# Performance work log

Hardware: AMD Instinct MI355X
Metric: run time of the kernel (lower is better)

Reference implementation:

```python
import jax, jax.numpy as jnp
import numpy as np

N_HEAD = 8
HEAD_DIM = 64
DIM = 512
INNER = N_HEAD * HEAD_DIM
ATT_THRESHOLD = 1e-4
SCALE = HEAD_DIM ** -0.5


def setup_inputs() -> dict:
    key = jax.random.key(0)
    ks = jax.random.split(key, 7)
    b, n, dn = 2, 2048, 2048
    fr = jax.random.normal(ks[0], (b, n, DIM), dtype=jnp.float32)
    dt = jax.random.normal(ks[1], (b, dn, DIM), dtype=jnp.float32)
    s = DIM ** -0.5
    Wq = jax.random.normal(ks[2], (DIM, INNER), dtype=jnp.float32) * s
    Wk = jax.random.normal(ks[3], (DIM, INNER), dtype=jnp.float32) * s
    Wv = jax.random.normal(ks[4], (DIM, INNER), dtype=jnp.float32) * s
    Wo = jax.random.normal(ks[5], (INNER, DIM), dtype=jnp.float32) * (INNER ** -0.5)
    bo = jax.random.normal(ks[6], (DIM,), dtype=jnp.float32) * 0.01
    return {"fr": fr, "dt": dt, "Wq": Wq, "Wk": Wk, "Wv": Wv, "Wo": Wo, "bo": bo}


def reference(fr, dt, Wq, Wk, Wv, Wo, bo):
    b, n, _ = fr.shape
    dn = dt.shape[1]
    # projections -> [b, seq, n_head, head_dim]
    q = (fr @ Wq).reshape(b, n, N_HEAD, HEAD_DIM)
    k = (dt @ Wk).reshape(b, dn, N_HEAD, HEAD_DIM)
    v = (dt @ Wv).reshape(b, dn, N_HEAD, HEAD_DIM)
    # full attention matrix [b, h, n, dn]
    scores = jnp.einsum('bihd,bjhd->bhij', q, k) * SCALE
    attn = jax.nn.softmax(scores, axis=-1)
    # torch .clip(t) with one positional arg clamps the MIN: max(attn, t)
    attn = jnp.maximum(attn, ATT_THRESHOLD) - ATT_THRESHOLD
    attn = attn / jnp.sum(attn, axis=-1, keepdims=True)
    out = jnp.einsum('bhij,bjhd->bihd', attn, v).reshape(b, n, INNER)
    return out @ Wo + bo
```

## Files before the change

kernel.cpp:

```cpp
#include <hip/hip_runtime.h>
#include <hip/hip_bf16.h>

#define BB 2
#define SEQ 2048
#define NHEAD 8
#define HD 64
#define ATT_T 1e-4f
#define QSCALE 0.18033688011112042f

typedef short s16x8 __attribute__((ext_vector_type(8)));
typedef float f32x16 __attribute__((ext_vector_type(16)));

#define MFMA32(a, b, c) __builtin_amdgcn_mfma_f32_32x32x16_bf16((a), (b), (c), 0, 0, 0)
#define EXP2(x) __builtin_amdgcn_exp2f(x)
#define SB0() __builtin_amdgcn_sched_barrier(0)
#define WAITVM0() __builtin_amdgcn_s_waitcnt(0x0F70)
#define WAITVM4() __builtin_amdgcn_s_waitcnt(0x0F74)
#define WAITVM8() __builtin_amdgcn_s_waitcnt(0x0F78)

__device__ __forceinline__ unsigned short bfr(float x) {
  __hip_bfloat16 h = __float2bfloat16(x);
  return __builtin_bit_cast(unsigned short, h);
}
__device__ __forceinline__ unsigned int packbf(float a, float b) {
  return (unsigned int)bfr(a) | ((unsigned int)bfr(b) << 16);
}
__device__ __forceinline__ unsigned int permpack(float a, float b) {
  return __builtin_amdgcn_perm(__builtin_bit_cast(unsigned int, b),
                               __builtin_bit_cast(unsigned int, a), 0x07060302u);
}
__device__ __forceinline__ void async16(const void* g, void* l) {
  __builtin_amdgcn_global_load_lds(
      (const __attribute__((address_space(1))) unsigned int*)g,
      (__attribute__((address_space(3))) unsigned int*)l, 16, 0, 0);
}

__global__ __launch_bounds__(256) void prep(const float* __restrict__ fr,
                                            const float* __restrict__ dt,
                                            const float* __restrict__ w0,
                                            const float* __restrict__ w1,
                                            const float* __restrict__ w2,
                                            const float* __restrict__ w3,
                                            unsigned short* __restrict__ frB,
                                            unsigned short* __restrict__ dtB,
                                            unsigned short* __restrict__ o0,
                                            unsigned short* __restrict__ o1,
                                            unsigned short* __restrict__ o2,
                                            unsigned short* __restrict__ o3) {
  __shared__ float tle[64][65];
  const int bid = blockIdx.x;
  if (bid < 4096) {
    const float* x = bid < 2048 ? fr : dt;
    unsigned short* y = bid < 2048 ? frB : dtB;
    size_t i = ((size_t)(bid & 2047) * 256 + threadIdx.x) * 4;
    float4 v = *(const float4*)(x + i);
    uint2 p;
    p.x = packbf(v.x, v.y);
    p.y = packbf(v.z, v.w);
    *(uint2*)(y + i) = p;
    return;
  }
  const int idx = bid - 4096;
  const int z = idx >> 6;
  const float* W = z == 0 ? w0 : z == 1 ? w1 : z == 2 ? w2 : w3;
  unsigned short* WT = z == 0 ? o0 : z == 1 ? o1 : z == 2 ? o2 : o3;
  const int r0 = ((idx >> 3) & 7) * 64, c0 = (idx & 7) * 64;
  const int tr = threadIdx.x >> 4;
  const int tc = threadIdx.x & 15;
  #pragma unroll
  for (int i = 0; i < 4; i++) {
    int r = tr + i * 16;
    float4 v = *(const float4*)(W + (size_t)(r0 + r) * 512 + c0 + tc * 4);
    tle[r][tc * 4 + 0] = v.x;
    tle[r][tc * 4 + 1] = v.y;
    tle[r][tc * 4 + 2] = v.z;
    tle[r][tc * 4 + 3] = v.w;
  }
  __syncthreads();
  #pragma unroll
  for (int i = 0; i < 4; i++) {
    int c = tr + i * 16;
    int rr = tc * 4;
    uint2 p;
    p.x = packbf(tle[rr + 0][c], tle[rr + 1][c]);
    p.y = packbf(tle[rr + 2][c], tle[rr + 3][c]);
    *(uint2*)(WT + (size_t)(c0 + c) * 512 + r0 + rr) = p;
  }
}

__device__ __forceinline__ void gemm_core_bk64(const unsigned short* __restrict__ A,
                                               const unsigned short* __restrict__ BT,
                                               unsigned short* smem, int m0, int n0,
                                               int w, int lane, f32x16 (&acc)[2]) {
  unsigned short* Asm = smem;
  unsigned short* Bsm = smem + 8192;
  const int l31 = lane & 31, lh = lane >> 5;

  auto stage = [&](int kt, int buf) {
    const int k0 = kt * 64;
    #pragma unroll
    for (int i = 0; i < 2; i++) {
      int r = w * 2 + i, g = r >> 2, ks = r & 3;
      async16(A + (size_t)(m0 + g * 32 + l31) * 512 + k0 + ks * 16 + lh * 8,
              Asm + buf * 4096 + r * 512);
    }
    #pragma unroll
    for (int i = 0; i < 4; i++) {
      int r = w * 4 + i, gn = r >> 2, ks = r & 3;
      async16(BT + (size_t)(n0 + gn * 32 + l31) * 512 + k0 + ks * 16 + lh * 8,
              Bsm + buf * 8192 + r * 512);
    }
  };

  stage(0, 0);
  for (int kt = 0; kt < 8; ++kt) {
    __syncthreads();
    if (kt + 1 < 8) stage(kt + 1, (kt + 1) & 1);
    const int buf = kt & 1;
    const unsigned short* as = Asm + buf * 4096 + (w & 1) * 2048;
    const unsigned short* bs = Bsm + buf * 8192 + (w >> 1) * 4096;
    #pragma unroll
    for (int ks = 0; ks < 4; ++ks) {
      s16x8 af = *(const s16x8*)(as + ks * 512 + lane * 8);
      s16x8 b0 = *(const s16x8*)(bs + ks * 512 + lane * 8);
      s16x8 b1 = *(const s16x8*)(bs + 2048 + ks * 512 + lane * 8);
      acc[0] = MFMA32(af, b0, acc[0]);
      acc[1] = MFMA32(af, b1, acc[1]);
    }
  }
}

__global__ __launch_bounds__(256) void gemm_qkv(const unsigned short* __restrict__ frB,
                                                const unsigned short* __restrict__ dtB,
                                                const unsigned short* __restrict__ WqT,
                                                const unsigned short* __restrict__ WkT,
                                                const unsigned short* __restrict__ WvT,
                                                unsigned short* __restrict__ Qp,
                                                unsigned short* __restrict__ Kp,
                                                unsigned short* __restrict__ VTp) {
  __shared__ __align__(16) unsigned short smem[24576];
  const int tid = threadIdx.x, lane = tid & 63, w = tid >> 6;
  const int l31 = lane & 31, lh = lane >> 5;
  const int m0 = blockIdx.y * 64, n0 = blockIdx.x * 128;
  const int z = blockIdx.z;
  const unsigned short* A = z == 0 ? frB : dtB;
  const unsigned short* BT = z == 0 ? WqT : (z == 1 ? WkT : WvT);
  unsigned short* OP = z == 0 ? Qp : (z == 1 ? Kp : VTp);
  const float scale = z == 0 ? QSCALE : 1.0f;

  f32x16 acc[2];
  #pragma unroll
  for (int j = 0; j < 2; j++)
    #pragma unroll
    for (int r = 0; r < 16; r++) acc[j][r] = 0.f;

  gemm_core_bk64(A, BT, smem, m0, n0, w, lane, acc);

  const int wm = (w & 1) * 32, wn = (w >> 1) * 64;
  const int bb = m0 >> 11, s0 = m0 & 2047;
  __syncthreads();
  if (z <= 1) {
    #pragma unroll
    for (int j = 0; j < 2; j++)
      #pragma unroll
      for (int r = 0; r < 16; r++) {
        int mm = wm + (r & 3) + 8 * (r >> 2) + 4 * lh;
        int nn = wn + j * 32 + l31;
        smem[mm * 136 + nn] = bfr(acc[j][r] * scale);
      }
    __syncthreads();
    #pragma unroll
    for (int it = 0; it < 4; ++it) {
      int c = tid + it * 256;
      int mm = c >> 4, seg = c & 15;
      uint4 vdat = *(const uint4*)(smem + mm * 136 + seg * 8);
      int n = n0 + seg * 8, h = n >> 6, d = n & 63;
      *(uint4*)(OP + ((size_t)((bb * NHEAD + h) * SEQ + s0 + mm)) * HD + d) = vdat;
    }
  } else {
    #pragma unroll
    for (int j = 0; j < 2; j++)
      #pragma unroll
      for (int r = 0; r < 16; r += 2) {
        int mm = wm + (r & 3) + 8 * (r >> 2) + 4 * lh;
        int nn = wn + j * 32 + l31;
        *(unsigned int*)(smem + nn * 72 + mm) = packbf(acc[j][r], acc[j][r + 1]);
      }
    __syncthreads();
    #pragma unroll
    for (int it = 0; it < 4; ++it) {
      int c = tid + it * 256;
      int nn = c >> 3, seg = c & 7;
      uint4 vdat = *(const uint4*)(smem + nn * 72 + seg * 8);
      int n = n0 + nn, h = n >> 6, d = n & 63;
      *(uint4*)(OP + ((size_t)((bb * NHEAD + h) * HD + d)) * SEQ + s0 + seg * 8) = vdat;
    }
  }
}

__global__ __launch_bounds__(256) void gemm_out(const unsigned short* __restrict__ A,
                                                const unsigned short* __restrict__ BT,
                                                const float* __restrict__ bias,
                                                float* __restrict__ O) {
  __shared__ __align__(16) unsigned short smem[24576];
  const int tid = threadIdx.x, lane = tid & 63, w = tid >> 6;
  const int l31 = lane & 31, lh = lane >> 5;
  const int m0 = blockIdx.y * 64, n0 = blockIdx.x * 128;

  f32x16 acc[2];
  #pragma unroll
  for (int j = 0; j < 2; j++)
    #pragma unroll
    for (int r = 0; r < 16; r++) acc[j][r] = 0.f;

  gemm_core_bk64(A, BT, smem, m0, n0, w, lane, acc);

  const int wm = (w & 1) * 32, wn = (w >> 1) * 64;
  #pragma unroll
  for (int j = 0; j < 2; j++) {
    float bv = bias[n0 + wn + j * 32 + l31];
    #pragma unroll
    for (int r = 0; r < 16; r++) {
      int mm = wm + (r & 3) + 8 * (r >> 2) + 4 * lh;
      O[(size_t)(m0 + mm) * 512 + n0 + wn + j * 32 + l31] = acc[j][r] + bv;
    }
  }
}

__global__ __launch_bounds__(256, 2) void attn_mfma(const unsigned short* __restrict__ Q,
                                                    const unsigned short* __restrict__ K,
                                                    const unsigned short* __restrict__ VT,
                                                    unsigned short* __restrict__ O) {
  __shared__ __align__(16) unsigned short arena[4][8192];
  __shared__ float larr[4][64];
  __shared__ float warr[4][64];

  const int tid = threadIdx.x;
  const int lane = tid & 63;
  const int w = tid >> 6;
  const int l31 = lane & 31, lh = lane >> 5;

  const int bid = blockIdx.x;
  const int g = bid & 7, j = bid >> 3;
  const int bh = g * 2 + (j >> 5);
  const int qt = j & 31;

  const unsigned short* Qh = Q + (size_t)bh * SEQ * HD;
  const unsigned short* Kh = K + (size_t)bh * SEQ * HD;
  const unsigned short* VTh = VT + (size_t)bh * HD * SEQ;

  s16x8 qf[2][4];
  #pragma unroll
  for (int q2 = 0; q2 < 2; q2++)
    #pragma unroll
    for (int t = 0; t < 4; t++)
      qf[q2][t] = *(const s16x8*)(Qh + (size_t)(qt * 64 + q2 * 32 + l31) * HD + 16 * t + 8 * lh);

  unsigned short* kbuf = &arena[w][0];
  unsigned short* vbuf = &arena[w][4096];
  const int kbase = w * 512;

  auto stageK = [&](int c, int slot) {
    const unsigned short* base = Kh + (size_t)(kbase + c * 32 + l31) * HD + lh * 8;
    #pragma unroll
    for (int tt = 0; tt < 4; tt++)
      async16(base + tt * 16, kbuf + slot * 2048 + tt * 512);
  };
  auto stageV = [&](int c, int slot) {
    #pragma unroll
    for (int dh = 0; dh < 2; dh++)
      #pragma unroll
      for (int kc = 0; kc < 2; kc++)
        async16(VTh + (size_t)(dh * 32 + l31) * SEQ + kbase + c * 32 + kc * 16 + lh * 8,
                vbuf + slot * 2048 + (dh * 2 + kc) * 512);
  };

  float lsum[2] = {0.f, 0.f};
  f32x16 scp[2];

  auto accum_l = [&]() {
    #pragma unroll
    for (int q2 = 0; q2 < 2; q2++) {
      float s0 = 0.f, s1 = 0.f, s2 = 0.f, s3 = 0.f;
      #pragma unroll
      for (int r = 0; r < 4; r++) {
        s0 += EXP2(scp[q2][r]);
        s1 += EXP2(scp[q2][4 + r]);
        s2 += EXP2(scp[q2][8 + r]);
        s3 += EXP2(scp[q2][12 + r]);
      }
      lsum[q2] += (s0 + s1) + (s2 + s3);
    }
  };

  stageK(0, 0);
  for (int c = 0; c < 16; ++c) {
    const int slot = c & 1;
    if (c + 1 < 16) stageK(c + 1, slot ^ 1);
    if (c > 0) accum_l();
    if (c + 1 < 16) { WAITVM4(); } else { WAITVM0(); }
    SB0();
    s16x8 kf[4];
    #pragma unroll
    for (int tt = 0; tt < 4; tt++)
      kf[tt] = *(const s16x8*)(kbuf + slot * 2048 + tt * 512 + lane * 8);
    #pragma unroll
    for (int q2 = 0; q2 < 2; q2++) {
      f32x16 sc;
      #pragma unroll
      for (int r = 0; r < 16; r++) sc[r] = 0.f;
      #pragma unroll
      for (int tt = 0; tt < 4; tt++) sc = MFMA32(kf[tt], qf[q2][tt], sc);
      scp[q2] = sc;
    }
  }
  accum_l();
  #pragma unroll
  for (int q2 = 0; q2 < 2; q2++) lsum[q2] += __shfl_xor(lsum[q2], 32);
  if (lh == 0) { larr[w][l31] = lsum[0]; larr[w][32 + l31] = lsum[1]; }
  __syncthreads();
  float tl[2];
  #pragma unroll
  for (int q2 = 0; q2 < 2; q2++)
    tl[q2] = ATT_T * (larr[0][q2 * 32 + l31] + larr[1][q2 * 32 + l31] +
                      larr[2][q2 * 32 + l31] + larr[3][q2 * 32 + l31]);

  f32x16 acc[2][2];
  #pragma unroll
  for (int q2 = 0; q2 < 2; q2++)
    #pragma unroll
    for (int dh = 0; dh < 2; dh++)
      #pragma unroll
      for (int r = 0; r < 16; r++) acc[q2][dh][r] = 0.f;
  float wacc[2] = {0.f, 0.f};
  s16x8 vfp[2][2];

  auto softmax_pv = [&]() {
    s16x8 pf[2][2];
    #pragma unroll
    for (int q2 = 0; q2 < 2; q2++) {
      uint2 quads[4];
      #pragma unroll
      for (int gq = 0; gq < 4; gq++) {
        float u0 = fmaxf(EXP2(scp[q2][4 * gq + 0]) - tl[q2], 0.f);
        float u1 = fmaxf(EXP2(scp[q2][4 * gq + 1]) - tl[q2], 0.f);
        float u2 = fmaxf(EXP2(scp[q2][4 * gq + 2]) - tl[q2], 0.f);
        float u3 = fmaxf(EXP2(scp[q2][4 * gq + 3]) - tl[q2], 0.f);
        wacc[q2] += (u0 + u1) + (u2 + u3);
        quads[gq].x = permpack(u0, u1);
        quads[gq].y = permpack(u2, u3);
      }
      #pragma unroll
      for (int tp = 0; tp < 2; tp++) {
        uint2 ea, eb;
        ea.x = (unsigned)__shfl_xor((int)quads[2 * tp].x, 32);
        ea.y = (unsigned)__shfl_xor((int)quads[2 * tp].y, 32);
        eb.x = (unsigned)__shfl_xor((int)quads[2 * tp + 1].x, 32);
        eb.y = (unsigned)__shfl_xor((int)quads[2 * tp + 1].y, 32);
        uint4 fr;
        if (lh == 0) { fr.x = quads[2 * tp].x; fr.y = quads[2 * tp].y; fr.z = ea.x; fr.w = ea.y; }
        else         { fr.x = eb.x; fr.y = eb.y; fr.z = quads[2 * tp + 1].x; fr.w = quads[2 * tp + 1].y; }
        pf[q2][tp] = __builtin_bit_cast(s16x8, fr);
      }
    }
    #pragma unroll
    for (int q2 = 0; q2 < 2; q2++)
      #pragma unroll
      for (int dh = 0; dh < 2; dh++) {
        acc[q2][dh] = MFMA32(pf[q2][0], vfp[dh][0], acc[q2][dh]);
        acc[q2][dh] = MFMA32(pf[q2][1], vfp[dh][1], acc[q2][dh]);
      }
  };

  stageK(0, 0);
  stageV(0, 0);
  for (int c = 0; c < 16; ++c) {
    const int slot = c & 1;
    if (c + 1 < 16) { stageK(c + 1, slot ^ 1); stageV(c + 1, slot ^ 1); }
    if (c > 0) softmax_pv();
    if (c + 1 < 16) { WAITVM8(); } else { WAITVM0(); }
    SB0();
    s16x8 kf[4];
    #pragma unroll
    for (int tt = 0; tt < 4; tt++)
      kf[tt] = *(const s16x8*)(kbuf + slot * 2048 + tt * 512 + lane * 8);
    #pragma unroll
    for (int dh = 0; dh < 2; dh++)
      #pragma unroll
      for (int kc = 0; kc < 2; kc++)
        vfp[dh][kc] = *(const s16x8*)(vbuf + slot * 2048 + (dh * 2 + kc) * 512 + lane * 8);
    #pragma unroll
    for (int q2 = 0; q2 < 2; q2++) {
      f32x16 sc;
      #pragma unroll
      for (int r = 0; r < 16; r++) sc[r] = 0.f;
      #pragma unroll
      for (int tt = 0; tt < 4; tt++) sc = MFMA32(kf[tt], qf[q2][tt], sc);
      scp[q2] = sc;
    }
  }
  softmax_pv();

  #pragma unroll
  for (int q2 = 0; q2 < 2; q2++) wacc[q2] += __shfl_xor(wacc[q2], 32);
  if (lh == 0) { warr[w][l31] = wacc[0]; warr[w][32 + l31] = wacc[1]; }
  __syncthreads();

  float* plane0 = (float*)&arena[0][0];
  float* plane1 = (float*)&arena[2][0];

  if (w >= 2) {
    float* pl = (w == 2) ? plane0 : plane1;
    #pragma unroll
    for (int q2 = 0; q2 < 2; q2++)
      #pragma unroll
      for (int dh = 0; dh < 2; dh++)
        #pragma unroll
        for (int r = 0; r < 16; r++) {
          int ql = q2 * 32 + (r & 3) + 8 * (r >> 2) + 4 * lh;
          pl[ql * 64 + dh * 32 + l31] = acc[q2][dh][r];
        }
  }
  __syncthreads();
  if (w < 2) {
    float* pl = (w == 0) ? plane0 : plane1;
    #pragma unroll
    for (int q2 = 0; q2 < 2; q2++)
      #pragma unroll
      for (int dh = 0; dh < 2; dh++)
        #pragma unroll
        for (int r = 0; r < 16; r++) {
          int ql = q2 * 32 + (r & 3) + 8 * (r >> 2) + 4 * lh;
          acc[q2][dh][r] += pl[ql * 64 + dh * 32 + l31];
        }
  }
  __syncthreads();
  if (w == 1) {
    #pragma unroll
    for (int q2 = 0; q2 < 2; q2++)
      #pragma unroll
      for (int dh = 0; dh < 2; dh++)
        #pragma unroll
        for (int r = 0; r < 16; r++) {
          int ql = q2 * 32 + (r & 3) + 8 * (r >> 2) + 4 * lh;
          plane0[ql * 64 + dh * 32 + l31] = acc[q2][dh][r];
        }
  }
  __syncthreads();
  unsigned short* otile = &arena[2][0];
  if (w == 0) {
    #pragma unroll
    for (int q2 = 0; q2 < 2; q2++)
      #pragma unroll
      for (int dh = 0; dh < 2; dh++)
        #pragma unroll
        for (int r = 0; r < 16; r++) {
          int ql = q2 * 32 + (r & 3) + 8 * (r >> 2) + 4 * lh;
          float wt = warr[0][ql] + warr[1][ql] + warr[2][ql] + warr[3][ql];
          float v = (acc[q2][dh][r] + plane0[ql * 64 + dh * 32 + l31]) / wt;
          otile[ql * 64 + dh * 32 + l31] = bfr(v);
        }
  }
  __syncthreads();
  const int b = bh >> 3, h = bh & 7;
  #pragma unroll
  for (int it = 0; it < 2; ++it) {
    int c2 = tid + it * 256;
    int mm = c2 >> 3, seg = c2 & 7;
    uint4 vdat = *(const uint4*)(otile + mm * 64 + seg * 8);
    *(uint4*)(O + ((size_t)(b * SEQ + qt * 64 + mm)) * 512 + h * HD + seg * 8) = vdat;
  }
}

extern "C" void kernel_launch(void* const* d_in, const int* in_sizes, int n_in,
                              void* d_out, int out_size, void* d_ws, size_t ws_size,
                              hipStream_t stream) {
  const float* fr = (const float*)d_in[0];
  const float* dt = (const float*)d_in[1];
  const float* Wq = (const float*)d_in[2];
  const float* Wk = (const float*)d_in[3];
  const float* Wv = (const float*)d_in[4];
  const float* Wo = (const float*)d_in[5];
  const float* bo = (const float*)d_in[6];
  float* out = (float*)d_out;

  const size_t planeE = (size_t)BB * SEQ * 512;
  const size_t wE = 512 * 512;
  unsigned short* p = (unsigned short*)d_ws;
  unsigned short* frB = p; p += planeE;
  unsigned short* dtB = p; p += planeE;
  unsigned short* WqT = p; p += wE;
  unsigned short* WkT = p; p += wE;
  unsigned short* WvT = p; p += wE;
  unsigned short* WoT = p; p += wE;
  unsigned short* Qp  = p; p += planeE;
  unsigned short* Kp  = p; p += planeE;
  unsigned short* VTp = p; p += planeE;
  unsigned short* aoB = p; p += planeE;

  prep<<<4352, 256, 0, stream>>>(fr, dt, Wq, Wk, Wv, Wo, frB, dtB, WqT, WkT, WvT, WoT);

  gemm_qkv<<<dim3(4, 64, 3), 256, 0, stream>>>(frB, dtB, WqT, WkT, WvT, Qp, Kp, VTp);

  attn_mfma<<<BB * NHEAD * 32, 256, 0, stream>>>(Qp, Kp, VTp, aoB);

  gemm_out<<<dim3(4, 64), 256, 0, stream>>>(aoB, WoT, bo, out);
}
```

Baseline: 166.1 us.

## Cache exp scores in registers as bf16 to skip recomputing QK^T in second pass

The attention kernel now computes QK^T and exp2 only once. It packs the exponentials as bf16 into a 128-register array and reuses them in the second pass, which previously reloaded K and redid the score MFMAs. The query tile per block drops from 64 to 32 rows, which doubles the grid and halves LDS use. This raises register pressure sharply and may hurt occupancy or cause spills. Rounding to bf16 before the threshold subtraction also changes numerics slightly.

```diff
diff --git a/kernel.cpp b/kernel.cpp
--- a/kernel.cpp
+++ b/kernel.cpp
@@ -16,7 +16,6 @@
 #define SB0() __builtin_amdgcn_sched_barrier(0)
 #define WAITVM0() __builtin_amdgcn_s_waitcnt(0x0F70)
 #define WAITVM4() __builtin_amdgcn_s_waitcnt(0x0F74)
-#define WAITVM8() __builtin_amdgcn_s_waitcnt(0x0F78)
 
 __device__ __forceinline__ unsigned short bfr(float x) {
   __hip_bfloat16 h = __float2bfloat16(x);
@@ -28,6 +27,12 @@
 __device__ __forceinline__ unsigned int permpack(float a, float b) {
   return __builtin_amdgcn_perm(__builtin_bit_cast(unsigned int, b),
                                __builtin_bit_cast(unsigned int, a), 0x07060302u);
+}
+__device__ __forceinline__ float unpack_lo(unsigned int p) {
+  return __builtin_bit_cast(float, p << 16);
+}
+__device__ __forceinline__ float unpack_hi(unsigned int p) {
+  return __builtin_bit_cast(float, p & 0xFFFF0000u);
 }
 __device__ __forceinline__ void async16(const void* g, void* l) {
   __builtin_amdgcn_global_load_lds(
@@ -231,9 +236,9 @@
                                                     const unsigned short* __restrict__ K,
                                                     const unsigned short* __restrict__ VT,
                                                     unsigned short* __restrict__ O) {
-  __shared__ __align__(16) unsigned short arena[4][8192];
-  __shared__ float larr[4][64];
-  __shared__ float warr[4][64];
+  __shared__ __align__(16) unsigned short arena[4][2][2048];
+  __shared__ float larr[4][32];
+  __shared__ float warr[4][32];
 
   const int tid = threadIdx.x;
   const int lane = tid & 63;
@@ -242,29 +247,25 @@
 
   const int bid = blockIdx.x;
   const int g = bid & 7, j = bid >> 3;
-  const int bh = g * 2 + (j >> 5);
-  const int qt = j & 31;
+  const int bh = g * 2 + (j >> 6);
+  const int qt = j & 63;
 
   const unsigned short* Qh = Q + (size_t)bh * SEQ * HD;
   const unsigned short* Kh = K + (size_t)bh * SEQ * HD;
   const unsigned short* VTh = VT + (size_t)bh * HD * SEQ;
 
-  s16x8 qf[2][4];
-  #pragma unroll
-  for (int q2 = 0; q2 < 2; q2++)
-    #pragma unroll
-    for (int t = 0; t < 4; t++)
-      qf[q2][t] = *(const s16x8*)(Qh + (size_t)(qt * 64 + q2 * 32 + l31) * HD + 16 * t + 8 * lh);
-
-  unsigned short* kbuf = &arena[w][0];
-  unsigned short* vbuf = &arena[w][4096];
+  s16x8 qf[4];
+  #pragma unroll
+  for (int t = 0; t < 4; t++)
+    qf[t] = *(const s16x8*)(Qh + (size_t)(qt * 32 + l31) * HD + 16 * t + 8 * lh);
+
   const int kbase = w * 512;
 
   auto stageK = [&](int c, int slot) {
     const unsigned short* base = Kh + (size_t)(kbase + c * 32 + l31) * HD + lh * 8;
     #pragma unroll
     for (int tt = 0; tt < 4; tt++)
-      async16(base + tt * 16, kbuf + slot * 2048 + tt * 512);
+      async16(base + tt * 16, &arena[w][slot][tt * 512]);
   };
   auto stageV = [&](int c, int slot) {
     #pragma unroll
@@ -272,203 +273,153 @@
       #pragma unroll
       for (int kc = 0; kc < 2; kc++)
         async16(VTh + (size_t)(dh * 32 + l31) * SEQ + kbase + c * 32 + kc * 16 + lh * 8,
-                vbuf + slot * 2048 + (dh * 2 + kc) * 512);
+                &arena[w][slot][(dh * 2 + kc) * 512]);
   };
 
-  float lsum[2] = {0.f, 0.f};
-  f32x16 scp[2];
-
-  auto accum_l = [&]() {
-    #pragma unroll
-    for (int q2 = 0; q2 < 2; q2++) {
-      float s0 = 0.f, s1 = 0.f, s2 = 0.f, s3 = 0.f;
-      #pragma unroll
-      for (int r = 0; r < 4; r++) {
-        s0 += EXP2(scp[q2][r]);
-        s1 += EXP2(scp[q2][4 + r]);
-        s2 += EXP2(scp[q2][8 + r]);
-        s3 += EXP2(scp[q2][12 + r]);
-      }
-      lsum[q2] += (s0 + s1) + (s2 + s3);
-    }
-  };
-
+  unsigned int P[16][8];
+
+  float ls0 = 0.f, ls1 = 0.f, ls2 = 0.f, ls3 = 0.f;
   stageK(0, 0);
+  #pragma unroll 16
   for (int c = 0; c < 16; ++c) {
     const int slot = c & 1;
     if (c + 1 < 16) stageK(c + 1, slot ^ 1);
-    if (c > 0) accum_l();
+    else stageV(0, 0);
+    WAITVM4();
+    SB0();
+    s16x8 kf[4];
+    #pragma unroll
+    for (int tt = 0; tt < 4; tt++)
+      kf[tt] = *(const s16x8*)&arena[w][slot][tt * 512 + lane * 8];
+    f32x16 sc;
+    #pragma unroll
+    for (int r = 0; r < 16; r++) sc[r] = 0.f;
+    #pragma unroll
+    for (int tt = 0; tt < 4; tt++) sc = MFMA32(kf[tt], qf[tt], sc);
+    #pragma unroll
+    for (int gq = 0; gq < 4; gq++) {
+      float e0 = EXP2(sc[4 * gq + 0]);
+      float e1 = EXP2(sc[4 * gq + 1]);
+      float e2 = EXP2(sc[4 * gq + 2]);
+      float e3 = EXP2(sc[4 * gq + 3]);
+      ls0 += e0; ls1 += e1; ls2 += e2; ls3 += e3;
+      P[c][2 * gq + 0] = permpack(e0, e1);
+      P[c][2 * gq + 1] = permpack(e2, e3);
+    }
+  }
+  float lsum = (ls0 + ls1) + (ls2 + ls3);
+  lsum += __shfl_xor(lsum, 32);
+  if (lh == 0) larr[w][l31] = lsum;
+  __syncthreads();
+  const float tl = ATT_T * (larr[0][l31] + larr[1][l31] + larr[2][l31] + larr[3][l31]);
+
+  f32x16 acc[2];
+  #pragma unroll
+  for (int dh = 0; dh < 2; dh++)
+    #pragma unroll
+    for (int r = 0; r < 16; r++) acc[dh][r] = 0.f;
+  float wacc = 0.f;
+
+  #pragma unroll 16
+  for (int c = 0; c < 16; ++c) {
+    const int slot = c & 1;
+    if (c + 1 < 16) stageV(c + 1, slot ^ 1);
+    uint2 quads[4];
+    #pragma unroll
+    for (int gq = 0; gq < 4; gq++) {
+      unsigned pa = P[c][2 * gq + 0], pb = P[c][2 * gq + 1];
+      float u0 = fmaxf(unpack_lo(pa) - tl, 0.f);
+      float u1 = fmaxf(unpack_hi(pa) - tl, 0.f);
+      float u2 = fmaxf(unpack_lo(pb) - tl, 0.f);
+      float u3 = fmaxf(unpack_hi(pb) - tl, 0.f);
+      wacc += (u0 + u1) + (u2 + u3);
+      quads[gq].x = permpack(u0, u1);
+      quads[gq].y = permpack(u2, u3);
+    }
+    s16x8 pf[2];
+    #pragma unroll
+    for (int tp = 0; tp < 2; tp++) {
+      unsigned sx = (lh == 0) ? quads[2 * tp + 1].x : quads[2 * tp].x;
+      unsigned sy = (lh == 0) ? quads[2 * tp + 1].y : quads[2 * tp].y;
+      unsigned rx = (unsigned)__shfl_xor((int)sx, 32);
+      unsigned ry = (unsigned)__shfl_xor((int)sy, 32);
+      uint4 fr;
+      if (lh == 0) { fr.x = quads[2 * tp].x; fr.y = quads[2 * tp].y; fr.z = rx; fr.w = ry; }
+      else         { fr.x = rx; fr.y = ry; fr.z = quads[2 * tp + 1].x; fr.w = quads[2 * tp + 1].y; }
+      pf[tp] = __builtin_bit_cast(s16x8, fr);
+    }
     if (c + 1 < 16) { WAITVM4(); } else { WAITVM0(); }
     SB0();
-    s16x8 kf[4];
-    #pragma unroll
-    for (int tt = 0; tt < 4; tt++)
-      kf[tt] = *(const s16x8*)(kbuf + slot * 2048 + tt * 512 + lane * 8);
-    #pragma unroll
-    for (int q2 = 0; q2 < 2; q2++) {
-      f32x16 sc;
-      #pragma unroll
-      for (int r = 0; r < 16; r++) sc[r] = 0.f;
-      #pragma unroll
-      for (int tt = 0; tt < 4; tt++) sc = MFMA32(kf[tt], qf[q2][tt], sc);
-      scp[q2] = sc;
-    }
-  }
-  accum_l();
-  #pragma unroll
-  for (int q2 = 0; q2 < 2; q2++) lsum[q2] += __shfl_xor(lsum[q2], 32);
-  if (lh == 0) { larr[w][l31] = lsum[0]; larr[w][32 + l31] = lsum[1]; }
-  __syncthreads();
-  float tl[2];
-  #pragma unroll
-  for (int q2 = 0; q2 < 2; q2++)
-    tl[q2] = ATT_T * (larr[0][q2 * 32 + l31] + larr[1][q2 * 32 + l31] +
-                      larr[2][q2 * 32 + l31] + larr[3][q2 * 32 + l31]);
-
-  f32x16 acc[2][2];
-  #pragma unroll
-  for (int q2 = 0; q2 < 2; q2++)
-    #pragma unroll
-    for (int dh = 0; dh < 2; dh++)
-      #pragma unroll
-      for (int r = 0; r < 16; r++) acc[q2][dh][r] = 0.f;
-  float wacc[2] = {0.f, 0.f};
-  s16x8 vfp[2][2];
-
-  auto softmax_pv = [&]() {
-    s16x8 pf[2][2];
-    #pragma unroll
-    for (int q2 = 0; q2 < 2; q2++) {
-      uint2 quads[4];
-      #pragma unroll
-      for (int gq = 0; gq < 4; gq++) {
-        float u0 = fmaxf(EXP2(scp[q2][4 * gq + 0]) - tl[q2], 0.f);
-        float u1 = fmaxf(EXP2(scp[q2][4 * gq + 1]) - tl[q2], 0.f);
-        float u2 = fmaxf(EXP2(scp[q2][4 * gq + 2]) - tl[q2], 0.f);
-        float u3 = fmaxf(EXP2(scp[q2][4 * gq + 3]) - tl[q2], 0.f);
-        wacc[q2] += (u0 + u1) + (u2 + u3);
-        quads[gq].x = permpack(u0, u1);
-        quads[gq].y = permpack(u2, u3);
-      }
-      #pragma unroll
-      for (int tp = 0; tp < 2; tp++) {
-        uint2 ea, eb;
-        ea.x = (unsigned)__shfl_xor((int)quads[2 * tp].x, 32);
-        ea.y = (unsigned)__shfl_xor((int)quads[2 * tp].y, 32);
-        eb.x = (unsigned)__shfl_xor((int)quads[2 * tp + 1].x, 32);
-        eb.y = (unsigned)__shfl_xor((int)quads[2 * tp + 1].y, 32);
-        uint4 fr;
-        if (lh == 0) { fr.x = quads[2 * tp].x; fr.y = quads[2 * tp].y; fr.z = ea.x; fr.w = ea.y; }
-        else         { fr.x = eb.x; fr.y = eb.y; fr.z = quads[2 * tp + 1].x; fr.w = quads[2 * tp + 1].y; }
-        pf[q2][tp] = __builtin_bit_cast(s16x8, fr);
-      }
-    }
-    #pragma unroll
-    for (int q2 = 0; q2 < 2; q2++)
-      #pragma unroll
-      for (int dh = 0; dh < 2; dh++) {
-        acc[q2][dh] = MFMA32(pf[q2][0], vfp[dh][0], acc[q2][dh]);
-        acc[q2][dh] = MFMA32(pf[q2][1], vfp[dh][1], acc[q2][dh]);
-      }
-  };
-
-  stageK(0, 0);
-  stageV(0, 0);
-  for (int c = 0; c < 16; ++c) {
-    const int slot = c & 1;
-    if (c + 1 < 16) { stageK(c + 1, slot ^ 1); stageV(c + 1, slot ^ 1); }
-    if (c > 0) softmax_pv();
-    if (c + 1 < 16) { WAITVM8(); } else { WAITVM0(); }
-    SB0();
-    s16x8 kf[4];
-    #pragma unroll
-    for (int tt = 0; tt < 4; tt++)
-      kf[tt] = *(const s16x8*)(kbuf + slot * 2048 + tt * 512 + lane * 8);
+    s16x8 vf[2][2];
     #pragma unroll
     for (int dh = 0; dh < 2; dh++)
       #pragma unroll
       for (int kc = 0; kc < 2; kc++)
-        vfp[dh][kc] = *(const s16x8*)(vbuf + slot * 2048 + (dh * 2 + kc) * 512 + lane * 8);
-    #pragma unroll
-    for (int q2 = 0; q2 < 2; q2++) {
-      f32x16 sc;
-      #pragma unroll
-      for (int r = 0; r < 16; r++) sc[r] = 0.f;
-      #pragma unroll
-      for (int tt = 0; tt < 4; tt++) sc = MFMA32(kf[tt], qf[q2][tt], sc);
-      scp[q2] = sc;
-    }
-  }
-  softmax_pv();
-
-  #pragma unroll
-  for (int q2 = 0; q2 < 2; q2++) wacc[q2] += __shfl_xor(wacc[q2], 32);
-  if (lh == 0) { warr[w][l31] = wacc[0]; warr[w][32 + l31] = wacc[1]; }
-  __syncthreads();
-
-  float* plane0 = (float*)&arena[0][0];
-  float* plane1 = (float*)&arena[2][0];
+        vf[dh][kc] = *(const s16x8*)&arena[w][slot][(dh * 2 + kc) * 512 + lane * 8];
+    #pragma unroll
+    for (int dh = 0; dh < 2; dh++) {
+      acc[dh] = MFMA32(pf[0], vf[dh][0], acc[dh]);
+      acc[dh] = MFMA32(pf[1], vf[dh][1], acc[dh]);
+    }
+  }
+
+  wacc += __shfl_xor(wacc, 32);
+  if (lh == 0) warr[w][l31] = wacc;
+  __syncthreads();
+
+  float* plane0 = (float*)&arena[0][0][0];
+  float* plane1 = (float*)&arena[1][0][0];
+  unsigned short* otile = &arena[2][0][0];
 
   if (w >= 2) {
     float* pl = (w == 2) ? plane0 : plane1;
     #pragma unroll
-    for (int q2 = 0; q2 < 2; q2++)
-      #pragma unroll
-      for (int dh = 0; dh < 2; dh++)
-        #pragma unroll
-        for (int r = 0; r < 16; r++) {
-          int ql = q2 * 32 + (r & 3) + 8 * (r >> 2) + 4 * lh;
-          pl[ql * 64 + dh * 32 + l31] = acc[q2][dh][r];
-        }
+    for (int dh = 0; dh < 2; dh++)
+      #pragma unroll
+      for (int r = 0; r < 16; r++) {
+        int ql = (r & 3) + 8 * (r >> 2) + 4 * lh;
+        pl[ql * 64 + dh * 32 + l31] = acc[dh][r];
+      }
   }
   __syncthreads();
   if (w < 2) {
     float* pl = (w == 0) ? plane0 : plane1;
     #pragma unroll
-    for (int q2 = 0; q2 < 2; q2++)
-      #pragma unroll
-      for (int dh = 0; dh < 2; dh++)
-        #pragma unroll
-        for (int r = 0; r < 16; r++) {
-          int ql = q2 * 32 + (r & 3) + 8 * (r >> 2) + 4 * lh;
-          acc[q2][dh][r] += pl[ql * 64 + dh * 32 + l31];
-        }
+    for (int dh = 0; dh < 2; dh++)
+      #pragma unroll
+      for (int r = 0; r < 16; r++) {
+        int ql = (r & 3) + 8 * (r >> 2) + 4 * lh;
+        acc[dh][r] += pl[ql * 64 + dh * 32 + l31];
+      }
   }
   __syncthreads();
   if (w == 1) {
     #pragma unroll
-    for (int q2 = 0; q2 < 2; q2++)
-      #pragma unroll
-      for (int dh = 0; dh < 2; dh++)
-        #pragma unroll
-        for (int r = 0; r < 16; r++) {
-          int ql = q2 * 32 + (r & 3) + 8 * (r >> 2) + 4 * lh;
-          plane0[ql * 64 + dh * 32 + l31] = acc[q2][dh][r];
-        }
-  }
-  __syncthreads();
-  unsigned short* otile = &arena[2][0];
+    for (int dh = 0; dh < 2; dh++)
+      #pragma unroll
+      for (int r = 0; r < 16; r++) {
+        int ql = (r & 3) + 8 * (r >> 2) + 4 * lh;
+        plane0[ql * 64 + dh * 32 + l31] = acc[dh][r];
+      }
+  }
+  __syncthreads();
   if (w == 0) {
     #pragma unroll
-    for (int q2 = 0; q2 < 2; q2++)
-      #pragma unroll
-      for (int dh = 0; dh < 2; dh++)
-        #pragma unroll
-        for (int r = 0; r < 16; r++) {
-          int ql = q2 * 32 + (r & 3) + 8 * (r >> 2) + 4 * lh;
-          float wt = warr[0][ql] + warr[1][ql] + warr[2][ql] + warr[3][ql];
-          float v = (acc[q2][dh][r] + plane0[ql * 64 + dh * 32 + l31]) / wt;
-          otile[ql * 64 + dh * 32 + l31] = bfr(v);
-        }
+    for (int dh = 0; dh < 2; dh++)
+      #pragma unroll
+      for (int r = 0; r < 16; r++) {
+        int ql = (r & 3) + 8 * (r >> 2) + 4 * lh;
+        float wt = warr[0][ql] + warr[1][ql] + warr[2][ql] + warr[3][ql];
+        float v = (acc[dh][r] + plane0[ql * 64 + dh * 32 + l31]) / wt;
+        otile[ql * 64 + dh * 32 + l31] = bfr(v);
+      }
   }
   __syncthreads();
   const int b = bh >> 3, h = bh & 7;
-  #pragma unroll
-  for (int it = 0; it < 2; ++it) {
-    int c2 = tid + it * 256;
-    int mm = c2 >> 3, seg = c2 & 7;
+  {
+    int mm = tid >> 3, seg = tid & 7;
     uint4 vdat = *(const uint4*)(otile + mm * 64 + seg * 8);
-    *(uint4*)(O + ((size_t)(b * SEQ + qt * 64 + mm)) * 512 + h * HD + seg * 8) = vdat;
+    *(uint4*)(O + ((size_t)(b * SEQ + qt * 32 + mm)) * 512 + h * HD + seg * 8) = vdat;
   }
 }
 
@@ -502,7 +453,7 @@
 
   gemm_qkv<<<dim3(4, 64, 3), 256, 0, stream>>>(frB, dtB, WqT, WkT, WvT, Qp, Kp, VTp);
 
-  attn_mfma<<<BB * NHEAD * 32, 256, 0, stream>>>(Qp, Kp, VTp, aoB);
+  attn_mfma<<<BB * NHEAD * 64, 256, 0, stream>>>(Qp, Kp, VTp, aoB);
 
   gemm_out<<<dim3(4, 64), 256, 0, stream>>>(aoB, WoT, bo, out);
 }
```

New measurement: 216.7 us. +30.5%, slower.

## Fuse fp32-to-bf16 input conversion into QKV GEMM and shrink output GEMM tile

Applied to the files above, without the earlier changes.

The separate activation conversion pass is removed. gemm_qkv now loads fp32 fr/dt tiles straight into registers, packs them to bf16 and writes them into shared memory, with a one-stage register prefetch, so the bf16 activation copies are no longer written to or read from global memory. The prep kernel becomes a weight-only transpose kernel. gemm_out switches to 64x64 tiles, doubling its block count to improve occupancy on the small output GEMM. The cost is that the A operand now uses synchronous loads plus register conversion instead of async direct-to-LDS copies, and each fp32 row is re-converted by every N-block that reads it.

```diff
diff --git a/kernel.cpp b/kernel.cpp
--- a/kernel.cpp
+++ b/kernel.cpp
@@ -35,36 +35,18 @@
       (__attribute__((address_space(3))) unsigned int*)l, 16, 0, 0);
 }
 
-__global__ __launch_bounds__(256) void prep(const float* __restrict__ fr,
-                                            const float* __restrict__ dt,
-                                            const float* __restrict__ w0,
-                                            const float* __restrict__ w1,
-                                            const float* __restrict__ w2,
-                                            const float* __restrict__ w3,
-                                            unsigned short* __restrict__ frB,
-                                            unsigned short* __restrict__ dtB,
-                                            unsigned short* __restrict__ o0,
-                                            unsigned short* __restrict__ o1,
-                                            unsigned short* __restrict__ o2,
-                                            unsigned short* __restrict__ o3) {
+__global__ __launch_bounds__(256) void convT(const float* __restrict__ w0,
+                                             const float* __restrict__ w1,
+                                             const float* __restrict__ w2,
+                                             const float* __restrict__ w3,
+                                             unsigned short* __restrict__ o0,
+                                             unsigned short* __restrict__ o1,
+                                             unsigned short* __restrict__ o2,
+                                             unsigned short* __restrict__ o3) {
   __shared__ float tle[64][65];
-  const int bid = blockIdx.x;
-  if (bid < 4096) {
-    const float* x = bid < 2048 ? fr : dt;
-    unsigned short* y = bid < 2048 ? frB : dtB;
-    size_t i = ((size_t)(bid & 2047) * 256 + threadIdx.x) * 4;
-    float4 v = *(const float4*)(x + i);
-    uint2 p;
-    p.x = packbf(v.x, v.y);
-    p.y = packbf(v.z, v.w);
-    *(uint2*)(y + i) = p;
-    return;
-  }
-  const int idx = bid - 4096;
-  const int z = idx >> 6;
-  const float* W = z == 0 ? w0 : z == 1 ? w1 : z == 2 ? w2 : w3;
-  unsigned short* WT = z == 0 ? o0 : z == 1 ? o1 : z == 2 ? o2 : o3;
-  const int r0 = ((idx >> 3) & 7) * 64, c0 = (idx & 7) * 64;
+  const float* W = blockIdx.z == 0 ? w0 : blockIdx.z == 1 ? w1 : blockIdx.z == 2 ? w2 : w3;
+  unsigned short* WT = blockIdx.z == 0 ? o0 : blockIdx.z == 1 ? o1 : blockIdx.z == 2 ? o2 : o3;
+  const int r0 = blockIdx.y * 64, c0 = blockIdx.x * 64;
   const int tr = threadIdx.x >> 4;
   const int tc = threadIdx.x & 15;
   #pragma unroll
@@ -88,50 +70,8 @@
   }
 }
 
-__device__ __forceinline__ void gemm_core_bk64(const unsigned short* __restrict__ A,
-                                               const unsigned short* __restrict__ BT,
-                                               unsigned short* smem, int m0, int n0,
-                                               int w, int lane, f32x16 (&acc)[2]) {
-  unsigned short* Asm = smem;
-  unsigned short* Bsm = smem + 8192;
-  const int l31 = lane & 31, lh = lane >> 5;
-
-  auto stage = [&](int kt, int buf) {
-    const int k0 = kt * 64;
-    #pragma unroll
-    for (int i = 0; i < 2; i++) {
-      int r = w * 2 + i, g = r >> 2, ks = r & 3;
-      async16(A + (size_t)(m0 + g * 32 + l31) * 512 + k0 + ks * 16 + lh * 8,
-              Asm + buf * 4096 + r * 512);
-    }
-    #pragma unroll
-    for (int i = 0; i < 4; i++) {
-      int r = w * 4 + i, gn = r >> 2, ks = r & 3;
-      async16(BT + (size_t)(n0 + gn * 32 + l31) * 512 + k0 + ks * 16 + lh * 8,
-              Bsm + buf * 8192 + r * 512);
-    }
-  };
-
-  stage(0, 0);
-  for (int kt = 0; kt < 8; ++kt) {
-    __syncthreads();
-    if (kt + 1 < 8) stage(kt + 1, (kt + 1) & 1);
-    const int buf = kt & 1;
-    const unsigned short* as = Asm + buf * 4096 + (w & 1) * 2048;
-    const unsigned short* bs = Bsm + buf * 8192 + (w >> 1) * 4096;
-    #pragma unroll
-    for (int ks = 0; ks < 4; ++ks) {
-      s16x8 af = *(const s16x8*)(as + ks * 512 + lane * 8);
-      s16x8 b0 = *(const s16x8*)(bs + ks * 512 + lane * 8);
-      s16x8 b1 = *(const s16x8*)(bs + 2048 + ks * 512 + lane * 8);
-      acc[0] = MFMA32(af, b0, acc[0]);
-      acc[1] = MFMA32(af, b1, acc[1]);
-    }
-  }
-}
-
-__global__ __launch_bounds__(256) void gemm_qkv(const unsigned short* __restrict__ frB,
-                                                const unsigned short* __restrict__ dtB,
+__global__ __launch_bounds__(256) void gemm_qkv(const float* __restrict__ frF,
+                                                const float* __restrict__ dtF,
                                                 const unsigned short* __restrict__ WqT,
                                                 const unsigned short* __restrict__ WkT,
                                                 const unsigned short* __restrict__ WvT,
@@ -139,22 +79,76 @@
                                                 unsigned short* __restrict__ Kp,
                                                 unsigned short* __restrict__ VTp) {
   __shared__ __align__(16) unsigned short smem[24576];
+  unsigned short* Asm = smem;
+  unsigned short* Bsm = smem + 8192;
   const int tid = threadIdx.x, lane = tid & 63, w = tid >> 6;
   const int l31 = lane & 31, lh = lane >> 5;
   const int m0 = blockIdx.y * 64, n0 = blockIdx.x * 128;
   const int z = blockIdx.z;
-  const unsigned short* A = z == 0 ? frB : dtB;
+  const float* A = z == 0 ? frF : dtF;
   const unsigned short* BT = z == 0 ? WqT : (z == 1 ? WkT : WvT);
   unsigned short* OP = z == 0 ? Qp : (z == 1 ? Kp : VTp);
   const float scale = z == 0 ? QSCALE : 1.0f;
 
+  const int arow = tid >> 2, aseg = tid & 3;
+  const float* Ap = A + (size_t)(m0 + arow) * 512 + aseg * 16;
+  const int aoff = (arow >> 5) * 2048 + aseg * 512 + (arow & 31) * 8;
+
+  auto stageB = [&](int kt, int buf) {
+    const int k0 = kt * 64;
+    #pragma unroll
+    for (int i = 0; i < 4; i++) {
+      int r = w * 4 + i, gn = r >> 2, ks = r & 3;
+      async16(BT + (size_t)(n0 + gn * 32 + l31) * 512 + k0 + ks * 16 + lh * 8,
+              Bsm + buf * 8192 + r * 512);
+    }
+  };
+  auto ldA = [&](int kt, float4* r4) {
+    #pragma unroll
+    for (int i = 0; i < 4; i++) r4[i] = *(const float4*)(Ap + kt * 64 + i * 4);
+  };
+  auto wrA = [&](int buf, const float4* r4) {
+    uint4 w0v, w1v;
+    w0v.x = packbf(r4[0].x, r4[0].y); w0v.y = packbf(r4[0].z, r4[0].w);
+    w0v.z = packbf(r4[1].x, r4[1].y); w0v.w = packbf(r4[1].z, r4[1].w);
+    w1v.x = packbf(r4[2].x, r4[2].y); w1v.y = packbf(r4[2].z, r4[2].w);
+    w1v.z = packbf(r4[3].x, r4[3].y); w1v.w = packbf(r4[3].z, r4[3].w);
+    *(uint4*)(Asm + buf * 4096 + aoff) = w0v;
+    *(uint4*)(Asm + buf * 4096 + aoff + 256) = w1v;
+  };
+
   f32x16 acc[2];
   #pragma unroll
   for (int j = 0; j < 2; j++)
     #pragma unroll
     for (int r = 0; r < 16; r++) acc[j][r] = 0.f;
 
-  gemm_core_bk64(A, BT, smem, m0, n0, w, lane, acc);
+  float4 areg[4];
+  ldA(0, areg);
+  stageB(0, 0);
+  wrA(0, areg);
+  ldA(1, areg);
+
+  for (int kt = 0; kt < 8; ++kt) {
+    __syncthreads();
+    if (kt + 1 < 8) {
+      const int nb = (kt + 1) & 1;
+      stageB(kt + 1, nb);
+      wrA(nb, areg);
+      if (kt + 2 < 8) ldA(kt + 2, areg);
+    }
+    const int buf = kt & 1;
+    const unsigned short* as = Asm + buf * 4096 + (w & 1) * 2048;
+    const unsigned short* bs = Bsm + buf * 8192 + (w >> 1) * 4096;
+    #pragma unroll
+    for (int ks = 0; ks < 4; ++ks) {
+      s16x8 af = *(const s16x8*)(as + ks * 512 + lane * 8);
+      s16x8 b0 = *(const s16x8*)(bs + ks * 512 + lane * 8);
+      s16x8 b1 = *(const s16x8*)(bs + 2048 + ks * 512 + lane * 8);
+      acc[0] = MFMA32(af, b0, acc[0]);
+      acc[1] = MFMA32(af, b1, acc[1]);
+    }
+  }
 
   const int wm = (w & 1) * 32, wn = (w >> 1) * 64;
   const int bb = m0 >> 11, s0 = m0 & 2047;
@@ -202,28 +196,50 @@
                                                 const unsigned short* __restrict__ BT,
                                                 const float* __restrict__ bias,
                                                 float* __restrict__ O) {
-  __shared__ __align__(16) unsigned short smem[24576];
+  __shared__ __align__(16) unsigned short smem[16384];
+  unsigned short* Asm = smem;
+  unsigned short* Bsm = smem + 8192;
   const int tid = threadIdx.x, lane = tid & 63, w = tid >> 6;
   const int l31 = lane & 31, lh = lane >> 5;
-  const int m0 = blockIdx.y * 64, n0 = blockIdx.x * 128;
-
-  f32x16 acc[2];
-  #pragma unroll
-  for (int j = 0; j < 2; j++)
-    #pragma unroll
-    for (int r = 0; r < 16; r++) acc[j][r] = 0.f;
-
-  gemm_core_bk64(A, BT, smem, m0, n0, w, lane, acc);
-
-  const int wm = (w & 1) * 32, wn = (w >> 1) * 64;
-  #pragma unroll
-  for (int j = 0; j < 2; j++) {
-    float bv = bias[n0 + wn + j * 32 + l31];
-    #pragma unroll
-    for (int r = 0; r < 16; r++) {
-      int mm = wm + (r & 3) + 8 * (r >> 2) + 4 * lh;
-      O[(size_t)(m0 + mm) * 512 + n0 + wn + j * 32 + l31] = acc[j][r] + bv;
-    }
+  const int m0 = blockIdx.y * 64, n0 = blockIdx.x * 64;
+
+  auto stage = [&](int kt, int buf) {
+    const int k0 = kt * 64;
+    #pragma unroll
+    for (int i = 0; i < 2; i++) {
+      int r = w * 2 + i, g = r >> 2, ks = r & 3;
+      async16(A + (size_t)(m0 + g * 32 + l31) * 512 + k0 + ks * 16 + lh * 8,
+              Asm + buf * 4096 + r * 512);
+      async16(BT + (size_t)(n0 + g * 32 + l31) * 512 + k0 + ks * 16 + lh * 8,
+              Bsm + buf * 4096 + r * 512);
+    }
+  };
+
+  f32x16 acc;
+  #pragma unroll
+  for (int r = 0; r < 16; r++) acc[r] = 0.f;
+
+  stage(0, 0);
+  for (int kt = 0; kt < 8; ++kt) {
+    __syncthreads();
+    if (kt + 1 < 8) stage(kt + 1, (kt + 1) & 1);
+    const int buf = kt & 1;
+    const unsigned short* as = Asm + buf * 4096 + (w & 1) * 2048;
+    const unsigned short* bs = Bsm + buf * 4096 + (w >> 1) * 2048;
+    #pragma unroll
+    for (int ks = 0; ks < 4; ++ks) {
+      s16x8 af = *(const s16x8*)(as + ks * 512 + lane * 8);
+      s16x8 bf = *(const s16x8*)(bs + ks * 512 + lane * 8);
+      acc = MFMA32(af, bf, acc);
+    }
+  }
+
+  const int wm = (w & 1) * 32, wn = (w >> 1) * 32;
+  float bv = bias[n0 + wn + l31];
+  #pragma unroll
+  for (int r = 0; r < 16; r++) {
+    int mm = wm + (r & 3) + 8 * (r >> 2) + 4 * lh;
+    O[(size_t)(m0 + mm) * 512 + n0 + wn + l31] = acc[r] + bv;
   }
 }
 
@@ -487,8 +503,6 @@
   const size_t planeE = (size_t)BB * SEQ * 512;
   const size_t wE = 512 * 512;
   unsigned short* p = (unsigned short*)d_ws;
-  unsigned short* frB = p; p += planeE;
-  unsigned short* dtB = p; p += planeE;
   unsigned short* WqT = p; p += wE;
   unsigned short* WkT = p; p += wE;
   unsigned short* WvT = p; p += wE;
@@ -498,11 +512,11 @@
   unsigned short* VTp = p; p += planeE;
   unsigned short* aoB = p; p += planeE;
 
-  prep<<<4352, 256, 0, stream>>>(fr, dt, Wq, Wk, Wv, Wo, frB, dtB, WqT, WkT, WvT, WoT);
-
-  gemm_qkv<<<dim3(4, 64, 3), 256, 0, stream>>>(frB, dtB, WqT, WkT, WvT, Qp, Kp, VTp);
+  convT<<<dim3(8, 8, 4), 256, 0, stream>>>(Wq, Wk, Wv, Wo, WqT, WkT, WvT, WoT);
+
+  gemm_qkv<<<dim3(4, 64, 3), 256, 0, stream>>>(fr, dt, WqT, WkT, WvT, Qp, Kp, VTp);
 
   attn_mfma<<<BB * NHEAD * 32, 256, 0, stream>>>(Qp, Kp, VTp, aoB);
 
-  gemm_out<<<dim3(4, 64), 256, 0, stream>>>(aoB, WoT, bo, out);
-}
+  gemm_out<<<dim3(8, 64), 256, 0, stream>>>(aoB, WoT, bo, out);
+}
```

New measurement: 162.8 us, median of 4. About the same (-2.0%).

## Use per-wave private LDS staging in projection GEMMs and shrink output GEMM tile

Applied to the files above, without the earlier changes.

Replaces the shared block-wide double-buffered GEMM core with per-wave private LDS slots, so each wave stages only its own A/B fragments and waits with vmcnt counters instead of __syncthreads barriers. BK drops to 32 with 16 k-steps. The output GEMM also moves to 64x64 tiles with one accumulator per wave, doubling its grid to add parallelism. The trade is duplicated A/B loads across waves and smaller MFMA work per stage. The unsynchronized LDS reuse relies on each wave consuming only its own slot.

```diff
diff --git a/kernel.cpp b/kernel.cpp
--- a/kernel.cpp
+++ b/kernel.cpp
@@ -16,6 +16,7 @@
 #define SB0() __builtin_amdgcn_sched_barrier(0)
 #define WAITVM0() __builtin_amdgcn_s_waitcnt(0x0F70)
 #define WAITVM4() __builtin_amdgcn_s_waitcnt(0x0F74)
+#define WAITVM6() __builtin_amdgcn_s_waitcnt(0x0F76)
 #define WAITVM8() __builtin_amdgcn_s_waitcnt(0x0F78)
 
 __device__ __forceinline__ unsigned short bfr(float x) {
@@ -88,48 +89,6 @@
   }
 }
 
-__device__ __forceinline__ void gemm_core_bk64(const unsigned short* __restrict__ A,
-                                               const unsigned short* __restrict__ BT,
-                                               unsigned short* smem, int m0, int n0,
-                                               int w, int lane, f32x16 (&acc)[2]) {
-  unsigned short* Asm = smem;
-  unsigned short* Bsm = smem + 8192;
-  const int l31 = lane & 31, lh = lane >> 5;
-
-  auto stage = [&](int kt, int buf) {
-    const int k0 = kt * 64;
-    #pragma unroll
-    for (int i = 0; i < 2; i++) {
-      int r = w * 2 + i, g = r >> 2, ks = r & 3;
-      async16(A + (size_t)(m0 + g * 32 + l31) * 512 + k0 + ks * 16 + lh * 8,
-              Asm + buf * 4096 + r * 512);
-    }
-    #pragma unroll
-    for (int i = 0; i < 4; i++) {
-      int r = w * 4 + i, gn = r >> 2, ks = r & 3;
-      async16(BT + (size_t)(n0 + gn * 32 + l31) * 512 + k0 + ks * 16 + lh * 8,
-              Bsm + buf * 8192 + r * 512);
-    }
-  };
-
-  stage(0, 0);
-  for (int kt = 0; kt < 8; ++kt) {
-    __syncthreads();
-    if (kt + 1 < 8) stage(kt + 1, (kt + 1) & 1);
-    const int buf = kt & 1;
-    const unsigned short* as = Asm + buf * 4096 + (w & 1) * 2048;
-    const unsigned short* bs = Bsm + buf * 8192 + (w >> 1) * 4096;
-    #pragma unroll
-    for (int ks = 0; ks < 4; ++ks) {
-      s16x8 af = *(const s16x8*)(as + ks * 512 + lane * 8);
-      s16x8 b0 = *(const s16x8*)(bs + ks * 512 + lane * 8);
-      s16x8 b1 = *(const s16x8*)(bs + 2048 + ks * 512 + lane * 8);
-      acc[0] = MFMA32(af, b0, acc[0]);
-      acc[1] = MFMA32(af, b1, acc[1]);
-    }
-  }
-}
-
 __global__ __launch_bounds__(256) void gemm_qkv(const unsigned short* __restrict__ frB,
                                                 const unsigned short* __restrict__ dtB,
                                                 const unsigned short* __restrict__ WqT,
@@ -138,7 +97,7 @@
                                                 unsigned short* __restrict__ Qp,
                                                 unsigned short* __restrict__ Kp,
                                                 unsigned short* __restrict__ VTp) {
-  __shared__ __align__(16) unsigned short smem[24576];
+  __shared__ __align__(16) unsigned short gar[4][6144];
   const int tid = threadIdx.x, lane = tid & 63, w = tid >> 6;
   const int l31 = lane & 31, lh = lane >> 5;
   const int m0 = blockIdx.y * 64, n0 = blockIdx.x * 128;
@@ -148,15 +107,47 @@
   unsigned short* OP = z == 0 ? Qp : (z == 1 ? Kp : VTp);
   const float scale = z == 0 ? QSCALE : 1.0f;
 
+  const int wm = (w & 1) * 32, wn = (w >> 1) * 64;
+
+  auto stage = [&](int kt, int slot) {
+    const int k0 = kt * 32;
+    unsigned short* dst = &gar[w][slot * 3072];
+    #pragma unroll
+    for (int ks = 0; ks < 2; ks++)
+      async16(A + (size_t)(m0 + wm + l31) * 512 + k0 + ks * 16 + lh * 8,
+              dst + ks * 512);
+    #pragma unroll
+    for (int gn = 0; gn < 2; gn++)
+      #pragma unroll
+      for (int ks = 0; ks < 2; ks++)
+        async16(BT + (size_t)(n0 + wn + gn * 32 + l31) * 512 + k0 + ks * 16 + lh * 8,
+                dst + 1024 + gn * 1024 + ks * 512);
+  };
+
   f32x16 acc[2];
   #pragma unroll
   for (int j = 0; j < 2; j++)
     #pragma unroll
     for (int r = 0; r < 16; r++) acc[j][r] = 0.f;
 
-  gemm_core_bk64(A, BT, smem, m0, n0, w, lane, acc);
-
-  const int wm = (w & 1) * 32, wn = (w >> 1) * 64;
+  stage(0, 0);
+  for (int kt = 0; kt < 16; ++kt) {
+    const int slot = kt & 1;
+    if (kt + 1 < 16) { stage(kt + 1, slot ^ 1); WAITVM6(); } else { WAITVM0(); }
+    SB0();
+    const unsigned short* as = &gar[w][slot * 3072];
+    const unsigned short* bs = as + 1024;
+    #pragma unroll
+    for (int ks = 0; ks < 2; ++ks) {
+      s16x8 af = *(const s16x8*)(as + ks * 512 + lane * 8);
+      s16x8 b0 = *(const s16x8*)(bs + ks * 512 + lane * 8);
+      s16x8 b1 = *(const s16x8*)(bs + 1024 + ks * 512 + lane * 8);
+      acc[0] = MFMA32(af, b0, acc[0]);
+      acc[1] = MFMA32(af, b1, acc[1]);
+    }
+  }
+
+  unsigned short* smem = &gar[0][0];
   const int bb = m0 >> 11, s0 = m0 & 2047;
   __syncthreads();
   if (z <= 1) {
@@ -202,28 +193,47 @@
                                                 const unsigned short* __restrict__ BT,
                                                 const float* __restrict__ bias,
                                                 float* __restrict__ O) {
-  __shared__ __align__(16) unsigned short smem[24576];
+  __shared__ __align__(16) unsigned short gar[4][4096];
   const int tid = threadIdx.x, lane = tid & 63, w = tid >> 6;
   const int l31 = lane & 31, lh = lane >> 5;
-  const int m0 = blockIdx.y * 64, n0 = blockIdx.x * 128;
-
-  f32x16 acc[2];
-  #pragma unroll
-  for (int j = 0; j < 2; j++)
-    #pragma unroll
-    for (int r = 0; r < 16; r++) acc[j][r] = 0.f;
-
-  gemm_core_bk64(A, BT, smem, m0, n0, w, lane, acc);
-
-  const int wm = (w & 1) * 32, wn = (w >> 1) * 64;
-  #pragma unroll
-  for (int j = 0; j < 2; j++) {
-    float bv = bias[n0 + wn + j * 32 + l31];
-    #pragma unroll
-    for (int r = 0; r < 16; r++) {
-      int mm = wm + (r & 3) + 8 * (r >> 2) + 4 * lh;
-      O[(size_t)(m0 + mm) * 512 + n0 + wn + j * 32 + l31] = acc[j][r] + bv;
-    }
+  const int m0 = blockIdx.y * 64, n0 = blockIdx.x * 64;
+  const int wm = (w & 1) * 32, wn = (w >> 1) * 32;
+
+  auto stage = [&](int kt, int slot) {
+    const int k0 = kt * 32;
+    unsigned short* dst = &gar[w][slot * 2048];
+    #pragma unroll
+    for (int ks = 0; ks < 2; ks++) {
+      async16(A + (size_t)(m0 + wm + l31) * 512 + k0 + ks * 16 + lh * 8,
+              dst + ks * 512);
+      async16(BT + (size_t)(n0 + wn + l31) * 512 + k0 + ks * 16 + lh * 8,
+              dst + 1024 + ks * 512);
+    }
+  };
+
+  f32x16 acc;
+  #pragma unroll
+  for (int r = 0; r < 16; r++) acc[r] = 0.f;
+
+  stage(0, 0);
+  for (int kt = 0; kt < 16; ++kt) {
+    const int slot = kt & 1;
+    if (kt + 1 < 16) { stage(kt + 1, slot ^ 1); WAITVM4(); } else { WAITVM0(); }
+    SB0();
+    const unsigned short* as = &gar[w][slot * 2048];
+    #pragma unroll
+    for (int ks = 0; ks < 2; ++ks) {
+      s16x8 af = *(const s16x8*)(as + ks * 512 + lane * 8);
+      s16x8 bf = *(const s16x8*)(as + 1024 + ks * 512 + lane * 8);
+      acc = MFMA32(af, bf, acc);
+    }
+  }
+
+  float bv = bias[n0 + wn + l31];
+  #pragma unroll
+  for (int r = 0; r < 16; r++) {
+    int mm = wm + (r & 3) + 8 * (r >> 2) + 4 * lh;
+    O[(size_t)(m0 + mm) * 512 + n0 + wn + l31] = acc[r] + bv;
   }
 }
 
@@ -504,5 +514,5 @@
 
   attn_mfma<<<BB * NHEAD * 32, 256, 0, stream>>>(Qp, Kp, VTp, aoB);
 
-  gemm_out<<<dim3(4, 64), 256, 0, stream>>>(aoB, WoT, bo, out);
-}
+  gemm_out<<<dim3(8, 64), 256, 0, stream>>>(aoB, WoT, bo, out);
+}
```

After: 187.4 us. 12.9% more time.
